# Kernel optimization log

Hardware: AMD Instinct MI355X
Metric: run time of the kernel (lower is better)

## Reference

```python
import jax, jax.numpy as jnp
import numpy as np

D_MODEL = 512
WINDOW = 128
N_HEADS = 8


def setup_inputs() -> dict:
    key = jax.random.key(0)
    k1, k2, k3, k4, k5 = jax.random.split(key, 5)
    B, S, D = 8, 4096, D_MODEL
    scale = 1.0 / np.sqrt(D)
    return {
        "x": jax.random.normal(k1, (B, S, D), dtype=jnp.float32),
        "in_proj_w": jax.random.normal(k2, (3 * D, D), dtype=jnp.float32) * scale,
        "in_proj_b": jax.random.normal(k3, (3 * D,), dtype=jnp.float32) * 0.02,
        "out_proj_w": jax.random.normal(k4, (D, D), dtype=jnp.float32) * scale,
        "out_proj_b": jax.random.normal(k5, (D,), dtype=jnp.float32) * 0.02,
    }


def reference(x, in_proj_w, in_proj_b, out_proj_w, out_proj_b):
    # Non-overlapping sliding-window MHA with shared weights per window.
    B, S, D = x.shape
    W = WINDOW
    H = N_HEADS
    hd = D // H
    nw = S // W  # S chosen divisible by window size

    xw = x.reshape(B, nw, W, D)
    # Fused QKV projection (torch in_proj_weight layout: [3D, D], y = x @ W^T + b)
    qkv = jnp.einsum("bnwd,ed->bnwe", xw, in_proj_w) + in_proj_b  # [B,nw,W,3D]
    q, k, v = jnp.split(qkv, 3, axis=-1)

    def to_heads(t):
        return t.reshape(B, nw, W, H, hd)

    q = to_heads(q) * (1.0 / np.sqrt(hd))
    k = to_heads(k)
    v = to_heads(v)

    # Block-diagonal attention: scores only within each window [B,nw,H,W,W]
    scores = jnp.einsum("bnqhd,bnkhd->bnhqk", q, k)
    attn = jax.nn.softmax(scores, axis=-1)
    ctx = jnp.einsum("bnhqk,bnkhd->bnqhd", attn, v)  # [B,nw,W,H,hd]
    ctx = ctx.reshape(B, S, D)

    out = jnp.einsum("bsd,ed->bse", ctx, out_proj_w) + out_proj_b
    return out
```

## Files before the change

kernel.cpp:

```cpp
#include <hip/hip_runtime.h>


typedef __bf16 bf16x8 __attribute__((ext_vector_type(8)));
typedef __bf16 bf16x4 __attribute__((ext_vector_type(4)));
typedef float  f32x4  __attribute__((ext_vector_type(4)));

#define MFMA16(a, b, c) __builtin_amdgcn_mfma_f32_16x16x32_bf16((a), (b), (c), 0, 0, 0)

__device__ __forceinline__ void gload_lds16(const __bf16* g, void* l) {
    __builtin_amdgcn_global_load_lds(
        (const __attribute__((address_space(1))) unsigned int*)g,
        (__attribute__((address_space(3))) unsigned int*)l, 16, 0, 0);
}

__device__ __forceinline__ void cvt8(const float* __restrict__ s,
                                     __bf16* __restrict__ d, long i) {
    const float4* s4 = reinterpret_cast<const float4*>(s);
    float4 a = s4[2 * i], b = s4[2 * i + 1];
    bf16x8 v;
    v[0] = (__bf16)a.x; v[1] = (__bf16)a.y; v[2] = (__bf16)a.z; v[3] = (__bf16)a.w;
    v[4] = (__bf16)b.x; v[5] = (__bf16)b.y; v[6] = (__bf16)b.z; v[7] = (__bf16)b.w;
    *reinterpret_cast<bf16x8*>(d + 8 * i) = v;
}

__global__ void convert_k(const float* __restrict__ x,
                          const float* __restrict__ w_in,
                          const float* __restrict__ w_out,
                          __bf16* __restrict__ x_bf,
                          __bf16* __restrict__ w_in_bf,
                          __bf16* __restrict__ w_out_bf)
{
    long i0 = (long)blockIdx.x * blockDim.x + threadIdx.x;
    long stride = (long)gridDim.x * blockDim.x;
    for (long i = i0; i < 16777216 / 8; i += stride) cvt8(x, x_bf, i);
    for (long i = i0; i < 786432 / 8;   i += stride) cvt8(w_in, w_in_bf, i);
    for (long i = i0; i < 262144 / 8;   i += stride) cvt8(w_out, w_out_bf, i);
}

template<int EPI, int NN>
__global__ __launch_bounds__(256)
void gemm128(const __bf16* __restrict__ A,
             const __bf16* __restrict__ Bw,
             const float* __restrict__ bias,
             void* __restrict__ Cq,
             __bf16* __restrict__ vT)
{
    __shared__ __bf16 Al[8192];
    __shared__ __bf16 Bl[8192];

    const int nwg = gridDim.x;
    const int chunk = nwg >> 3;
    const int bid = blockIdx.x;
    const int wg = (bid & 7) * chunk + (bid >> 3);
    const int nidx = wg % NN;
    const int midx = wg / NN;
    const long mbase = (long)midx * 128;
    const int colbase = nidx * 128;

    const int tid = threadIdx.x;
    const int w = tid >> 6, lane = tid & 63;
    const int lrow = lane & 15, hi = lane >> 4;
    const int srow = lane >> 3, sslot = lane & 7;
    const int sswz = sslot ^ (srow & 7);

    const __bf16* Ag = A + (mbase + w * 32 + srow) * 512 + sswz * 8;
    const __bf16* Bg = Bw + ((long)colbase + w * 32 + srow) * 512 + sswz * 8;
    char* Alc = (char*)Al + w * 4096;
    char* Blc = (char*)Bl + w * 4096;

    const int wm = w >> 1, wn = w & 1;

    f32x4 acc[4][4];
    #pragma unroll
    for (int rt = 0; rt < 4; ++rt)
        #pragma unroll
        for (int ct = 0; ct < 4; ++ct) acc[rt][ct] = (f32x4){0.f, 0.f, 0.f, 0.f};

    for (int k0 = 0; k0 < 512; k0 += 64) {
        #pragma unroll
        for (int i = 0; i < 4; ++i) {
            gload_lds16(Ag + (i * 8) * 512 + k0, Alc + i * 1024);
            gload_lds16(Bg + (i * 8) * 512 + k0, Blc + i * 1024);
        }
        __syncthreads();
        #pragma unroll
        for (int ks = 0; ks < 2; ++ks) {
            bf16x8 af[4], bfr[4];
            #pragma unroll
            for (int rt = 0; rt < 4; ++rt) {
                int row = 64 * wm + 16 * rt + lrow;
                af[rt] = *reinterpret_cast<const bf16x8*>(
                    (const char*)Al + row * 128 + ((ks * 64 + hi * 16) ^ ((row & 7) << 4)));
            }
            #pragma unroll
            for (int ct = 0; ct < 4; ++ct) {
                int row = 64 * wn + 16 * ct + lrow;
                bfr[ct] = *reinterpret_cast<const bf16x8*>(
                    (const char*)Bl + row * 128 + ((ks * 64 + hi * 16) ^ ((row & 7) << 4)));
            }
            #pragma unroll
            for (int rt = 0; rt < 4; ++rt)
                #pragma unroll
                for (int ct = 0; ct < 4; ++ct)
                    acc[rt][ct] = MFMA16(af[rt], bfr[ct], acc[rt][ct]);
        }
        __syncthreads();
    }

    if (EPI == 0) {
        const int region = colbase >> 9;
        if (region < 2) {
            __bf16* qk = (__bf16*)Cq;
            const float scale = (region == 0) ? 0.125f : 1.0f;
            #pragma unroll
            for (int ct = 0; ct < 4; ++ct) {
                int colg = colbase + 64 * wn + 16 * ct + lrow;
                float b = bias[colg];
                #pragma unroll
                for (int rt = 0; rt < 4; ++rt) {
                    long row = mbase + 64 * wm + 16 * rt + 4 * hi;
                    #pragma unroll
                    for (int r = 0; r < 4; ++r)
                        qk[(row + r) * 1024 + colg] = (__bf16)((acc[rt][ct][r] + b) * scale);
                }
            }
        } else {
            #pragma unroll
            for (int ct = 0; ct < 4; ++ct) {
                int colg = colbase + 64 * wn + 16 * ct + lrow;
                float b = bias[colg];
                int e2 = colg - 1024;
                int h = e2 >> 6, d = e2 & 63;
                #pragma unroll
                for (int rt = 0; rt < 4; ++rt) {
                    int tok0 = 64 * wm + 16 * rt + 4 * hi;
                    bf16x4 pk;
                    pk[0] = (__bf16)(acc[rt][ct][0] + b);
                    pk[1] = (__bf16)(acc[rt][ct][1] + b);
                    pk[2] = (__bf16)(acc[rt][ct][2] + b);
                    pk[3] = (__bf16)(acc[rt][ct][3] + b);
                    *reinterpret_cast<bf16x4*>(
                        vT + (((long)midx * 8 + h) * 64 + d) * 128 + tok0) = pk;
                }
            }
        }
    } else {
        float* out = (float*)Cq;
        #pragma unroll
        for (int ct = 0; ct < 4; ++ct) {
            int colg = colbase + 64 * wn + 16 * ct + lrow;
            float b = bias[colg];
            #pragma unroll
            for (int rt = 0; rt < 4; ++rt) {
                long row = mbase + 64 * wm + 16 * rt + 4 * hi;
                #pragma unroll
                for (int r = 0; r < 4; ++r)
                    out[(row + r) * 512 + colg] = acc[rt][ct][r] + b;
            }
        }
    }
}

__global__ __launch_bounds__(256)
void swa_attn(const __bf16* __restrict__ qk,
              const __bf16* __restrict__ vT,
              __bf16* __restrict__ ctx)
{
    __shared__ __bf16 p_lds[4][32][136];

    const int bid = blockIdx.x;
    const int win = bid >> 3, h = bid & 7;
    const int tid = threadIdx.x;
    const int w = tid >> 6, lane = tid & 63;
    const int lrow = lane & 15, hi = lane >> 4;
    const long tokb = (long)win * 128;

    bf16x8 qa[2][2];
    #pragma unroll
    for (int rt = 0; rt < 2; ++rt)
        #pragma unroll
        for (int ks = 0; ks < 2; ++ks)
            qa[rt][ks] = *reinterpret_cast<const bf16x8*>(
                qk + (tokb + 32 * w + 16 * rt + lrow) * 1024 + h * 64 + ks * 32 + hi * 8);

    f32x4 s[2][8];
    #pragma unroll
    for (int rt = 0; rt < 2; ++rt)
        #pragma unroll
        for (int ct = 0; ct < 8; ++ct) s[rt][ct] = (f32x4){0.f, 0.f, 0.f, 0.f};
    #pragma unroll
    for (int ks = 0; ks < 2; ++ks) {
        #pragma unroll
        for (int ct = 0; ct < 8; ++ct) {
            bf16x8 kb = *reinterpret_cast<const bf16x8*>(
                qk + (tokb + 16 * ct + lrow) * 1024 + 512 + h * 64 + ks * 32 + hi * 8);
            s[0][ct] = MFMA16(qa[0][ks], kb, s[0][ct]);
            s[1][ct] = MFMA16(qa[1][ks], kb, s[1][ct]);
        }
    }

    float inv[2][4];
    #pragma unroll
    for (int rt = 0; rt < 2; ++rt) {
        #pragma unroll
        for (int r = 0; r < 4; ++r) {
            float m = s[rt][0][r];
            #pragma unroll
            for (int ct = 1; ct < 8; ++ct) m = fmaxf(m, s[rt][ct][r]);
            m = fmaxf(m, __shfl_xor(m, 1));
            m = fmaxf(m, __shfl_xor(m, 2));
            m = fmaxf(m, __shfl_xor(m, 4));
            m = fmaxf(m, __shfl_xor(m, 8));
            float sum = 0.f;
            #pragma unroll
            for (int ct = 0; ct < 8; ++ct) {
                float e = __expf(s[rt][ct][r] - m);
                sum += e;
                p_lds[w][16 * rt + 4 * hi + r][16 * ct + lrow] = (__bf16)e;
            }
            sum += __shfl_xor(sum, 1);
            sum += __shfl_xor(sum, 2);
            sum += __shfl_xor(sum, 4);
            sum += __shfl_xor(sum, 8);
            inv[rt][r] = 1.f / sum;
        }
    }

    f32x4 o[2][4];
    #pragma unroll
    for (int rt = 0; rt < 2; ++rt)
        #pragma unroll
        for (int ct = 0; ct < 4; ++ct) o[rt][ct] = (f32x4){0.f, 0.f, 0.f, 0.f};
    const __bf16* vb = vT + ((long)win * 8 + h) * 64 * 128;
    #pragma unroll
    for (int kt = 0; kt < 4; ++kt) {
        bf16x8 pa0 = *reinterpret_cast<const bf16x8*>(&p_lds[w][lrow][32 * kt + 8 * hi]);
        bf16x8 pa1 = *reinterpret_cast<const bf16x8*>(&p_lds[w][16 + lrow][32 * kt + 8 * hi]);
        #pragma unroll
        for (int ct = 0; ct < 4; ++ct) {
            bf16x8 vf = *reinterpret_cast<const bf16x8*>(
                vb + (16 * ct + lrow) * 128 + 32 * kt + 8 * hi);
            o[0][ct] = MFMA16(pa0, vf, o[0][ct]);
            o[1][ct] = MFMA16(pa1, vf, o[1][ct]);
        }
    }

    #pragma unroll
    for (int rt = 0; rt < 2; ++rt)
        #pragma unroll
        for (int ct = 0; ct < 4; ++ct)
            #pragma unroll
            for (int r = 0; r < 4; ++r) {
                long tok = tokb + 32 * w + 16 * rt + 4 * hi + r;
                ctx[tok * 512 + h * 64 + 16 * ct + lrow] =
                    (__bf16)(o[rt][ct][r] * inv[rt][r]);
            }
}

extern "C" void kernel_launch(void* const* d_in, const int* in_sizes, int n_in,
                              void* d_out, int out_size, void* d_ws, size_t ws_size,
                              hipStream_t stream)
{
    const float* x     = (const float*)d_in[0];
    const float* w_in  = (const float*)d_in[1];
    const float* b_in  = (const float*)d_in[2];
    const float* w_out = (const float*)d_in[3];
    const float* b_out = (const float*)d_in[4];

    char* ws = (char*)d_ws;
    __bf16* x_bf     = (__bf16*)(ws);
    __bf16* ctx      = (__bf16*)(ws);
    __bf16* vT       = (__bf16*)(ws + 33554432);
    __bf16* w_in_bf  = (__bf16*)(ws + 67108864);
    __bf16* w_out_bf = (__bf16*)(ws + 68681728);
    __bf16* qk       = (__bf16*)d_out;

    convert_k<<<2048, 256, 0, stream>>>(x, w_in, w_out, x_bf, w_in_bf, w_out_bf);
    gemm128<0, 12><<<3072, 256, 0, stream>>>(x_bf, w_in_bf, b_in, (void*)qk, vT);
    swa_attn<<<2048, 256, 0, stream>>>(qk, vT, ctx);
    gemm128<1, 4><<<1024, 256, 0, stream>>>(ctx, w_out_bf, b_out, d_out, nullptr);
}
```

Before: 165.9 us.

## Use 256x256 GEMM tiles with a 4-stage async LDS pipeline

Replaces the 128x128 single-buffered GEMM with a 256x256-tile, 512-thread kernel. K is streamed in 32-wide slices through a 4-deep ring of LDS buffers, with vmcnt waits so global-to-LDS loads overlap the MFMA work. It also raises wave priority around the MFMA block and adds a new swizzle for 64-byte rows. Larger tiles give more reuse per load, but the output GEMM now launches only 256 workgroups, which may underfill the GPU and add tail effects.

```diff
diff --git a/kernel.cpp b/kernel.cpp
--- a/kernel.cpp
+++ b/kernel.cpp
@@ -6,6 +6,11 @@
 typedef float  f32x4  __attribute__((ext_vector_type(4)));
 
 #define MFMA16(a, b, c) __builtin_amdgcn_mfma_f32_16x16x32_bf16((a), (b), (c), 0, 0, 0)
+
+#define VMCNT(n) asm volatile("s_waitcnt vmcnt(" #n ")" ::: "memory")
+#define SBAR() do { __builtin_amdgcn_sched_barrier(0); \
+                    __builtin_amdgcn_s_barrier(); \
+                    __builtin_amdgcn_sched_barrier(0); } while (0)
 
 __device__ __forceinline__ void gload_lds16(const __bf16* g, void* l) {
     __builtin_amdgcn_global_load_lds(
@@ -38,15 +43,15 @@
 }
 
 template<int EPI, int NN>
-__global__ __launch_bounds__(256)
-void gemm128(const __bf16* __restrict__ A,
+__global__ __launch_bounds__(512, 2)
+void gemm256(const __bf16* __restrict__ A,
              const __bf16* __restrict__ Bw,
              const float* __restrict__ bias,
              void* __restrict__ Cq,
              __bf16* __restrict__ vT)
 {
-    __shared__ __bf16 Al[8192];
-    __shared__ __bf16 Bl[8192];
+    __shared__ __bf16 Al[4][8192];
+    __shared__ __bf16 Bl[4][8192];
 
     const int nwg = gridDim.x;
     const int chunk = nwg >> 3;
@@ -54,58 +59,77 @@
     const int wg = (bid & 7) * chunk + (bid >> 3);
     const int nidx = wg % NN;
     const int midx = wg / NN;
-    const long mbase = (long)midx * 128;
-    const int colbase = nidx * 128;
+    const long mbase = (long)midx * 256;
+    const int colbase = nidx * 256;
 
     const int tid = threadIdx.x;
     const int w = tid >> 6, lane = tid & 63;
     const int lrow = lane & 15, hi = lane >> 4;
-    const int srow = lane >> 3, sslot = lane & 7;
-    const int sswz = sslot ^ (srow & 7);
-
-    const __bf16* Ag = A + (mbase + w * 32 + srow) * 512 + sswz * 8;
-    const __bf16* Bg = Bw + ((long)colbase + w * 32 + srow) * 512 + sswz * 8;
-    char* Alc = (char*)Al + w * 4096;
-    char* Blc = (char*)Bl + w * 4096;
-
-    const int wm = w >> 1, wn = w & 1;
-
-    f32x4 acc[4][4];
-    #pragma unroll
-    for (int rt = 0; rt < 4; ++rt)
+    const int wm = w >> 2, wn = w & 3;
+
+    const int st_row = lane >> 2;
+    const int st_slot = lane & 3;
+    const int st_k = 8 * (st_slot ^ ((lane >> 3) & 3));
+    const int rd_off = 16 * (hi ^ ((lrow >> 1) & 3));
+
+    const __bf16* PA = A  + (mbase + w * 16 + st_row) * 512 + st_k;
+    const __bf16* PB = Bw + ((long)colbase + w * 16 + st_row) * 512 + st_k;
+    const int lds_w = w * 1024;
+
+    f32x4 acc[8][4];
+    #pragma unroll
+    for (int rt = 0; rt < 8; ++rt)
         #pragma unroll
         for (int ct = 0; ct < 4; ++ct) acc[rt][ct] = (f32x4){0.f, 0.f, 0.f, 0.f};
 
-    for (int k0 = 0; k0 < 512; k0 += 64) {
-        #pragma unroll
-        for (int i = 0; i < 4; ++i) {
-            gload_lds16(Ag + (i * 8) * 512 + k0, Alc + i * 1024);
-            gload_lds16(Bg + (i * 8) * 512 + k0, Blc + i * 1024);
-        }
-        __syncthreads();
-        #pragma unroll
-        for (int ks = 0; ks < 2; ++ks) {
-            bf16x8 af[4], bfr[4];
-            #pragma unroll
-            for (int rt = 0; rt < 4; ++rt) {
-                int row = 64 * wm + 16 * rt + lrow;
-                af[rt] = *reinterpret_cast<const bf16x8*>(
-                    (const char*)Al + row * 128 + ((ks * 64 + hi * 16) ^ ((row & 7) << 4)));
-            }
-            #pragma unroll
-            for (int ct = 0; ct < 4; ++ct) {
-                int row = 64 * wn + 16 * ct + lrow;
-                bfr[ct] = *reinterpret_cast<const bf16x8*>(
-                    (const char*)Bl + row * 128 + ((ks * 64 + hi * 16) ^ ((row & 7) << 4)));
-            }
-            #pragma unroll
-            for (int rt = 0; rt < 4; ++rt)
-                #pragma unroll
-                for (int ct = 0; ct < 4; ++ct)
-                    acc[rt][ct] = MFMA16(af[rt], bfr[ct], acc[rt][ct]);
-        }
-        __syncthreads();
-    }
+    auto stage = [&](int tt) {
+        const int sl = tt & 3;
+        const int kk = tt * 32;
+        char* As = (char*)Al[sl];
+        char* Bs = (char*)Bl[sl];
+        gload_lds16(PA + kk,             As + lds_w);
+        gload_lds16(PA + 128 * 512 + kk, As + 8192 + lds_w);
+        gload_lds16(PB + kk,             Bs + lds_w);
+        gload_lds16(PB + 128 * 512 + kk, Bs + 8192 + lds_w);
+    };
+
+    auto body = [&](int t) {
+        const char* As = (const char*)Al[t & 3];
+        const char* Bs = (const char*)Bl[t & 3];
+        bf16x8 af[8], bf[4];
+        #pragma unroll
+        for (int rt = 0; rt < 8; ++rt) {
+            int row = 128 * wm + 16 * rt + lrow;
+            af[rt] = *reinterpret_cast<const bf16x8*>(As + row * 64 + rd_off);
+        }
+        #pragma unroll
+        for (int ct = 0; ct < 4; ++ct) {
+            int row = 64 * wn + 16 * ct + lrow;
+            bf[ct] = *reinterpret_cast<const bf16x8*>(Bs + row * 64 + rd_off);
+        }
+        __builtin_amdgcn_s_setprio(1);
+        #pragma unroll
+        for (int rt = 0; rt < 8; ++rt)
+            #pragma unroll
+            for (int ct = 0; ct < 4; ++ct)
+                acc[rt][ct] = MFMA16(af[rt], bf[ct], acc[rt][ct]);
+        __builtin_amdgcn_s_setprio(0);
+    };
+
+    stage(0); stage(1); stage(2);
+    VMCNT(8);
+    SBAR();
+
+    #pragma unroll 1
+    for (int t = 0; t < 13; ++t) {
+        stage(t + 3);
+        body(t);
+        VMCNT(8);
+        SBAR();
+    }
+    body(13); VMCNT(4); SBAR();
+    body(14); VMCNT(0); SBAR();
+    body(15);
 
     if (EPI == 0) {
         const int region = colbase >> 9;
@@ -117,8 +141,8 @@
                 int colg = colbase + 64 * wn + 16 * ct + lrow;
                 float b = bias[colg];
                 #pragma unroll
-                for (int rt = 0; rt < 4; ++rt) {
-                    long row = mbase + 64 * wm + 16 * rt + 4 * hi;
+                for (int rt = 0; rt < 8; ++rt) {
+                    long row = mbase + 128 * wm + 16 * rt + 4 * hi;
                     #pragma unroll
                     for (int r = 0; r < 4; ++r)
                         qk[(row + r) * 1024 + colg] = (__bf16)((acc[rt][ct][r] + b) * scale);
@@ -132,15 +156,16 @@
                 int e2 = colg - 1024;
                 int h = e2 >> 6, d = e2 & 63;
                 #pragma unroll
-                for (int rt = 0; rt < 4; ++rt) {
-                    int tok0 = 64 * wm + 16 * rt + 4 * hi;
+                for (int rt = 0; rt < 8; ++rt) {
+                    long row = mbase + 128 * wm + 16 * rt + 4 * hi;
+                    int win = (int)(row >> 7), tok0 = (int)(row & 127);
                     bf16x4 pk;
                     pk[0] = (__bf16)(acc[rt][ct][0] + b);
                     pk[1] = (__bf16)(acc[rt][ct][1] + b);
                     pk[2] = (__bf16)(acc[rt][ct][2] + b);
                     pk[3] = (__bf16)(acc[rt][ct][3] + b);
                     *reinterpret_cast<bf16x4*>(
-                        vT + (((long)midx * 8 + h) * 64 + d) * 128 + tok0) = pk;
+                        vT + (((long)win * 8 + h) * 64 + d) * 128 + tok0) = pk;
                 }
             }
         }
@@ -151,8 +176,8 @@
             int colg = colbase + 64 * wn + 16 * ct + lrow;
             float b = bias[colg];
             #pragma unroll
-            for (int rt = 0; rt < 4; ++rt) {
-                long row = mbase + 64 * wm + 16 * rt + 4 * hi;
+            for (int rt = 0; rt < 8; ++rt) {
+                long row = mbase + 128 * wm + 16 * rt + 4 * hi;
                 #pragma unroll
                 for (int r = 0; r < 4; ++r)
                     out[(row + r) * 512 + colg] = acc[rt][ct][r] + b;
@@ -276,7 +301,7 @@
     __bf16* qk       = (__bf16*)d_out;
 
     convert_k<<<2048, 256, 0, stream>>>(x, w_in, w_out, x_bf, w_in_bf, w_out_bf);
-    gemm128<0, 12><<<3072, 256, 0, stream>>>(x_bf, w_in_bf, b_in, (void*)qk, vT);
+    gemm256<0, 6><<<768, 512, 0, stream>>>(x_bf, w_in_bf, b_in, (void*)qk, vT);
     swa_attn<<<2048, 256, 0, stream>>>(qk, vT, ctx);
-    gemm128<1, 4><<<1024, 256, 0, stream>>>(ctx, w_out_bf, b_out, d_out, nullptr);
-}
+    gemm256<1, 2><<<256, 512, 0, stream>>>(ctx, w_out_bf, b_out, d_out, nullptr);
+}
```

Measured after the change: 175.9 us. 1.06x slower.

## Pipeline GEMM K-loop with triple-buffered LDS and stage epilogue through LDS

Applied to the files above, without the earlier changes.

Changes the projection GEMM from a single-buffered 64-wide K step with two full barriers per iteration to a three-slot, 32-wide K ring buffer. Loads run two stages ahead and completion is tracked with explicit vmcnt waits. The MFMA block is raised in priority and an occupancy hint of 3 blocks is added. The QK and V-transpose epilogues now stage results in LDS and write coalesced 16-byte rows, replacing scattered 2-byte and 8-byte global stores. The trade-off is more LDS per block (48KB), the loss of the XOR swizzle on LDS reads (possible bank conflicts), and hand-written waitcnt logic that must stay correct.

```diff
diff --git a/kernel.cpp b/kernel.cpp
--- a/kernel.cpp
+++ b/kernel.cpp
@@ -2,10 +2,12 @@
 
 
 typedef __bf16 bf16x8 __attribute__((ext_vector_type(8)));
-typedef __bf16 bf16x4 __attribute__((ext_vector_type(4)));
 typedef float  f32x4  __attribute__((ext_vector_type(4)));
 
 #define MFMA16(a, b, c) __builtin_amdgcn_mfma_f32_16x16x32_bf16((a), (b), (c), 0, 0, 0)
+#define VMCNT_(n) asm volatile("s_waitcnt vmcnt(" #n ")" ::: "memory")
+#define VMCNT(n) VMCNT_(n)
+#define LGKM0() asm volatile("s_waitcnt lgkmcnt(0)" ::: "memory")
 
 __device__ __forceinline__ void gload_lds16(const __bf16* g, void* l) {
     __builtin_amdgcn_global_load_lds(
@@ -38,15 +40,14 @@
 }
 
 template<int EPI, int NN>
-__global__ __launch_bounds__(256)
+__global__ __launch_bounds__(256, 3)
 void gemm128(const __bf16* __restrict__ A,
              const __bf16* __restrict__ Bw,
              const float* __restrict__ bias,
              void* __restrict__ Cq,
              __bf16* __restrict__ vT)
 {
-    __shared__ __bf16 Al[8192];
-    __shared__ __bf16 Bl[8192];
+    __shared__ __align__(16) char smem[49152];
 
     const int nwg = gridDim.x;
     const int chunk = nwg >> 3;
@@ -60,92 +61,115 @@
     const int tid = threadIdx.x;
     const int w = tid >> 6, lane = tid & 63;
     const int lrow = lane & 15, hi = lane >> 4;
-    const int srow = lane >> 3, sslot = lane & 7;
-    const int sswz = sslot ^ (srow & 7);
-
-    const __bf16* Ag = A + (mbase + w * 32 + srow) * 512 + sswz * 8;
-    const __bf16* Bg = Bw + ((long)colbase + w * 32 + srow) * 512 + sswz * 8;
-    char* Alc = (char*)Al + w * 4096;
-    char* Blc = (char*)Bl + w * 4096;
-
     const int wm = w >> 1, wn = w & 1;
 
+    const int srow = lane >> 2, sk = lane & 3;
+    const __bf16* PA = A  + (mbase + 32 * w + srow) * 512 + sk * 8;
+    const __bf16* PB = Bw + ((long)colbase + 32 * w + srow) * 512 + sk * 8;
+
     f32x4 acc[4][4];
     #pragma unroll
     for (int rt = 0; rt < 4; ++rt)
         #pragma unroll
         for (int ct = 0; ct < 4; ++ct) acc[rt][ct] = (f32x4){0.f, 0.f, 0.f, 0.f};
 
-    for (int k0 = 0; k0 < 512; k0 += 64) {
-        #pragma unroll
-        for (int i = 0; i < 4; ++i) {
-            gload_lds16(Ag + (i * 8) * 512 + k0, Alc + i * 1024);
-            gload_lds16(Bg + (i * 8) * 512 + k0, Blc + i * 1024);
-        }
-        __syncthreads();
-        #pragma unroll
-        for (int ks = 0; ks < 2; ++ks) {
-            bf16x8 af[4], bfr[4];
-            #pragma unroll
-            for (int rt = 0; rt < 4; ++rt) {
-                int row = 64 * wm + 16 * rt + lrow;
-                af[rt] = *reinterpret_cast<const bf16x8*>(
-                    (const char*)Al + row * 128 + ((ks * 64 + hi * 16) ^ ((row & 7) << 4)));
-            }
+    auto stage = [&](int t, int slot) {
+        char* As = smem + slot * 16384;
+        char* Bs = As + 8192;
+        const int ko = t * 32;
+        #pragma unroll
+        for (int j = 0; j < 2; ++j) {
+            gload_lds16(PA + ko + j * 16 * 512, As + (32 * w + 16 * j) * 64);
+            gload_lds16(PB + ko + j * 16 * 512, Bs + (32 * w + 16 * j) * 64);
+        }
+    };
+
+    stage(0, 0); stage(1, 1);
+
+    #pragma unroll 1
+    for (int t = 0; t < 16; ++t) {
+        if (t < 15) { VMCNT(4); } else { VMCNT(0); }
+        LGKM0();
+        __builtin_amdgcn_s_barrier();
+        if (t < 14) {
+            int t2 = t + 2;
+            stage(t2, t2 - (t2 >= 15 ? 15 : (t2 >= 12 ? 12 : (t2 >= 9 ? 9 : (t2 >= 6 ? 6 : (t2 >= 3 ? 3 : 0))))));
+        }
+        const int slot = t - (t >= 15 ? 15 : (t >= 12 ? 12 : (t >= 9 ? 9 : (t >= 6 ? 6 : (t >= 3 ? 3 : 0)))));
+        const char* As = smem + slot * 16384;
+        const char* Bs = As + 8192;
+        bf16x8 af[4], bfr[4];
+        #pragma unroll
+        for (int i = 0; i < 4; ++i)
+            af[i] = *reinterpret_cast<const bf16x8*>(
+                As + (64 * wm + 16 * i + lrow) * 64 + hi * 16);
+        #pragma unroll
+        for (int ct = 0; ct < 4; ++ct)
+            bfr[ct] = *reinterpret_cast<const bf16x8*>(
+                Bs + (64 * wn + 16 * ct + lrow) * 64 + hi * 16);
+        __builtin_amdgcn_s_setprio(1);
+        #pragma unroll
+        for (int i = 0; i < 4; ++i)
+            #pragma unroll
+            for (int ct = 0; ct < 4; ++ct)
+                acc[i][ct] = MFMA16(af[i], bfr[ct], acc[i][ct]);
+        __builtin_amdgcn_s_setprio(0);
+    }
+    LGKM0();
+    __builtin_amdgcn_s_barrier();
+
+    if (EPI == 0) {
+        if (colbase < 1024) {
+            const float scale = (colbase < 512) ? 0.125f : 1.0f;
+            __bf16* qk = (__bf16*)Cq;
             #pragma unroll
             for (int ct = 0; ct < 4; ++ct) {
-                int row = 64 * wn + 16 * ct + lrow;
-                bfr[ct] = *reinterpret_cast<const bf16x8*>(
-                    (const char*)Bl + row * 128 + ((ks * 64 + hi * 16) ^ ((row & 7) << 4)));
-            }
-            #pragma unroll
-            for (int rt = 0; rt < 4; ++rt)
+                int col = 64 * wn + 16 * ct + lrow;
+                float b = bias[colbase + col];
                 #pragma unroll
-                for (int ct = 0; ct < 4; ++ct)
-                    acc[rt][ct] = MFMA16(af[rt], bfr[ct], acc[rt][ct]);
-        }
-        __syncthreads();
-    }
-
-    if (EPI == 0) {
-        const int region = colbase >> 9;
-        if (region < 2) {
-            __bf16* qk = (__bf16*)Cq;
-            const float scale = (region == 0) ? 0.125f : 1.0f;
+                for (int rt = 0; rt < 4; ++rt)
+                    #pragma unroll
+                    for (int r = 0; r < 4; ++r) {
+                        int row = 64 * wm + 16 * rt + 4 * hi + r;
+                        *reinterpret_cast<__bf16*>(smem + row * 288 + col * 2) =
+                            (__bf16)((acc[rt][ct][r] + b) * scale);
+                    }
+            }
+            LGKM0();
+            __builtin_amdgcn_s_barrier();
+            #pragma unroll
+            for (int i = 0; i < 8; ++i) {
+                int row = 16 * i + (tid >> 4);
+                bf16x8 v = *reinterpret_cast<const bf16x8*>(smem + row * 288 + (tid & 15) * 16);
+                *reinterpret_cast<bf16x8*>(
+                    qk + (mbase + row) * 1024 + colbase + (tid & 15) * 8) = v;
+            }
+        } else {
             #pragma unroll
             for (int ct = 0; ct < 4; ++ct) {
-                int colg = colbase + 64 * wn + 16 * ct + lrow;
-                float b = bias[colg];
+                int e = 64 * wn + 16 * ct + lrow;
+                float b = bias[colbase + e];
                 #pragma unroll
-                for (int rt = 0; rt < 4; ++rt) {
-                    long row = mbase + 64 * wm + 16 * rt + 4 * hi;
+                for (int rt = 0; rt < 4; ++rt)
                     #pragma unroll
-                    for (int r = 0; r < 4; ++r)
-                        qk[(row + r) * 1024 + colg] = (__bf16)((acc[rt][ct][r] + b) * scale);
-                }
-            }
-        } else {
-            #pragma unroll
-            for (int ct = 0; ct < 4; ++ct) {
-                int colg = colbase + 64 * wn + 16 * ct + lrow;
-                float b = bias[colg];
-                int e2 = colg - 1024;
-                int h = e2 >> 6, d = e2 & 63;
-                #pragma unroll
-                for (int rt = 0; rt < 4; ++rt) {
-                    int tok0 = 64 * wm + 16 * rt + 4 * hi;
-                    bf16x4 pk;
-                    pk[0] = (__bf16)(acc[rt][ct][0] + b);
-                    pk[1] = (__bf16)(acc[rt][ct][1] + b);
-                    pk[2] = (__bf16)(acc[rt][ct][2] + b);
-                    pk[3] = (__bf16)(acc[rt][ct][3] + b);
-                    *reinterpret_cast<bf16x4*>(
-                        vT + (((long)midx * 8 + h) * 64 + d) * 128 + tok0) = pk;
-                }
+                    for (int r = 0; r < 4; ++r) {
+                        int tok = 64 * wm + 16 * rt + 4 * hi + r;
+                        *reinterpret_cast<__bf16*>(smem + e * 288 + tok * 2) =
+                            (__bf16)(acc[rt][ct][r] + b);
+                    }
+            }
+            LGKM0();
+            __builtin_amdgcn_s_barrier();
+            #pragma unroll
+            for (int i = 0; i < 8; ++i) {
+                int e = 16 * i + (tid >> 4);
+                bf16x8 v = *reinterpret_cast<const bf16x8*>(smem + e * 288 + (tid & 15) * 16);
+                *reinterpret_cast<bf16x8*>(
+                    vT + (long)midx * 65536 + (colbase - 1024 + e) * 128 + (tid & 15) * 8) = v;
             }
         }
     } else {
-        float* out = (float*)Cq;
+        float* outp = (float*)Cq;
         #pragma unroll
         for (int ct = 0; ct < 4; ++ct) {
             int colg = colbase + 64 * wn + 16 * ct + lrow;
@@ -155,7 +179,7 @@
                 long row = mbase + 64 * wm + 16 * rt + 4 * hi;
                 #pragma unroll
                 for (int r = 0; r < 4; ++r)
-                    out[(row + r) * 512 + colg] = acc[rt][ct][r] + b;
+                    outp[(row + r) * 512 + colg] = acc[rt][ct][r] + b;
             }
         }
     }
```

New measurement: 163.0 us. No clear change (-1.7%).
